# Kernel tuning notes

Hardware: AMD Instinct MI355X
Metric: run time of the kernel (lower is better)

## Reference

```python
import jax, jax.numpy as jnp
import numpy as np


def setup_inputs() -> dict:
    key = jax.random.key(0)
    k1, k2 = jax.random.split(key)
    B, C, L, K = 32, 64, 4096, 512
    inputs = jax.random.normal(k1, (B, C, L), dtype=jnp.float32)
    # codebook init: uniform(-1/K, 1/K) as in the torch module
    embed = jax.random.uniform(k2, (K, C), dtype=jnp.float32, minval=-1.0 / K, maxval=1.0 / K)
    return {"inputs": inputs, "embed": embed}


def reference(inputs, embed):
    commitment_cost = 0.25
    b, c, l = inputs.shape
    K = embed.shape[0]
    # (B, C, L) -> (B*L, C)
    flat = jnp.transpose(inputs, (0, 2, 1)).reshape(-1, c)
    flat_sq = jnp.sum(flat * flat, axis=1, keepdims=True)            # (N, 1)
    embed_sq = jnp.sum(embed * embed, axis=1)                        # (K,)
    distances = flat_sq + embed_sq[None, :] - 2.0 * (flat @ embed.T)  # (N, K)
    encoding_indices = jnp.argmin(distances, axis=1)                 # (N,)
    encodings = jax.nn.one_hot(encoding_indices, K, dtype=flat.dtype)  # (N, K)
    # gather codewords (equivalent to one_hot @ embed) and restore (B, C, L)
    quantized = jnp.transpose(embed[encoding_indices].reshape(b, l, c), (0, 2, 1))
    e_latent_loss = jnp.mean((jax.lax.stop_gradient(quantized) - inputs) ** 2)
    q_latent_loss = jnp.mean((quantized - jax.lax.stop_gradient(inputs)) ** 2)
    loss = q_latent_loss + commitment_cost * e_latent_loss
    # straight-through estimator
    quantized_st = inputs + jax.lax.stop_gradient(quantized - inputs)
    avg_probs = jnp.mean(encodings, axis=0)                          # (K,)
    perplexity = jnp.exp(-jnp.sum(avg_probs * jnp.log(avg_probs + 1e-10)))
    return (loss, quantized_st, perplexity, embed, encoding_indices.reshape(b, l), encodings)
```

## Files before the change

### kernel.cpp

```cpp
#include <hip/hip_runtime.h>
#include <math.h>

#define B_DIM 32
#define C_DIM 64
#define L_DIM 4096
#define K_CB  512
#define N_ROWS (B_DIM * L_DIM)
#define Q_ELEMS (B_DIM * C_DIM * L_DIM)

#define OFF_LOSS  0
#define OFF_Q     1
#define OFF_PERP  (1 + Q_ELEMS)
#define OFF_EMBED (OFF_PERP + 1)
#define OFF_IDX   (OFF_EMBED + K_CB * C_DIM)
#define OFF_ENC   (OFF_IDX + N_ROWS)

#define TM 128
#define KC 128

using f4 = __attribute__((ext_vector_type(4))) float;
using f2 = __attribute__((ext_vector_type(2))) float;


__global__ void vq_init(const float* __restrict__ embed,
                        double* __restrict__ loss_ws,
                        int* __restrict__ hist,
                        float* __restrict__ esq,
                        float* __restrict__ out_embed) {
  const int t = threadIdx.x;
  if (t == 0) *loss_ws = 0.0;
  hist[t] = 0;
  const float* row = embed + (size_t)t * C_DIM;
  float s = 0.f;
#pragma unroll
  for (int c = 0; c < C_DIM; ++c) s = fmaf(row[c], row[c], s);
  esq[t] = s;
#pragma unroll
  for (int i = 0; i < K_CB * C_DIM / 512; ++i)
    out_embed[i * 512 + t] = embed[i * 512 + t];
}

__global__ __launch_bounds__(256) void vq_fused(
    const float* __restrict__ in, const float* __restrict__ embed,
    const float* __restrict__ esq_g, int* __restrict__ hist,
    double* __restrict__ loss_ws, float* __restrict__ out) {
  __shared__ float xT[C_DIM][TM];
  __shared__ float eT[KC][C_DIM];
  __shared__ int   idx_s[TM];
  __shared__ double red[256];

  const int tid = threadIdx.x;
  const int blk = blockIdx.x;
  const int b   = blk >> 5;
  const int l0  = (blk & 31) * TM;
  const float* xbase = in + (size_t)b * C_DIM * L_DIM + l0;

  {
    const int rr = (tid & 31) * 4;
    const int c0 = tid >> 5;
#pragma unroll
    for (int p = 0; p < 8; ++p) {
      const int c = c0 * 8 + p;
      const f4 v = *(const f4*)(xbase + (size_t)c * L_DIM + rr);
      *(f4*)&xT[c][rr] = v;
    }
  }
  __syncthreads();

  const int tx = tid & 15;
  const int ty = tid >> 4;

  float* fsq_tmp = &eT[0][0];
  if (tid < TM) {
    float s = 0.f;
#pragma unroll
    for (int c = 0; c < C_DIM; ++c) { const float v = xT[c][tid]; s = fmaf(v, v, s); }
    fsq_tmp[tid] = s;
  }
  __syncthreads();
  float fs[8];
#pragma unroll
  for (int i = 0; i < 8; ++i) fs[i] = fsq_tmp[ty * 8 + i];

  const int swz = (tx & 7) << 2;
  float rmin[8];
  int   ridx[8];
#pragma unroll
  for (int i = 0; i < 8; ++i) { rmin[i] = 3.402823466e38f; ridx[i] = 0; }

  for (int kc = 0; kc < K_CB / KC; ++kc) {
    const int k0 = kc * KC;
    __syncthreads();
    {
      const int cg  = (tid & 15) * 4;
      const int kk0 = tid >> 4;
#pragma unroll
      for (int p = 0; p < 8; ++p) {
        const int kk = kk0 + p * 16;
        const f4 v = *(const f4*)(embed + (size_t)(k0 + kk) * C_DIM + cg);
        const int cs = cg ^ (((kk >> 3) & 7) << 2);
        *(f4*)&eT[kk][cs] = v;
      }
    }
    __syncthreads();

    float qe[8];
#pragma unroll
    for (int j = 0; j < 8; ++j) qe[j] = esq_g[k0 + tx * 8 + j];

    float acc[8][8];
#pragma unroll
    for (int i = 0; i < 8; ++i)
#pragma unroll
      for (int j = 0; j < 8; ++j) acc[i][j] = 0.f;

#pragma unroll 2
    for (int c = 0; c < C_DIM; c += 4) {
      f4 xa[4], xb[4], ev[8];
#pragma unroll
      for (int cc = 0; cc < 4; ++cc) {
        xa[cc] = *(const f4*)&xT[c + cc][ty * 8];
        xb[cc] = *(const f4*)&xT[c + cc][ty * 8 + 4];
      }
      const int cb = c ^ swz;
#pragma unroll
      for (int j = 0; j < 8; ++j)
        ev[j] = *(const f4*)&eT[tx * 8 + j][cb];
#pragma unroll
      for (int cc = 0; cc < 4; ++cc) {
#pragma unroll
        for (int j = 0; j < 8; ++j) {
          const float e = ev[j][cc];
#pragma unroll
          for (int i = 0; i < 4; ++i) acc[i][j]     = fmaf(xa[cc][i], e, acc[i][j]);
#pragma unroll
          for (int i = 0; i < 4; ++i) acc[i + 4][j] = fmaf(xb[cc][i], e, acc[i + 4][j]);
        }
      }
    }

#pragma unroll
    for (int i = 0; i < 8; ++i) {
#pragma unroll
      for (int j = 0; j < 8; ++j) {
        const float d = fmaf(-2.0f, acc[i][j], fs[i] + qe[j]);
        const int k = k0 + tx * 8 + j;
        if (d < rmin[i]) { rmin[i] = d; ridx[i] = k; }
      }
    }
  }

#pragma unroll
  for (int off = 8; off; off >>= 1) {
#pragma unroll
    for (int i = 0; i < 8; ++i) {
      const float od = __shfl_xor(rmin[i], off, 16);
      const int   oi = __shfl_xor(ridx[i], off, 16);
      if (od < rmin[i] || (od == rmin[i] && oi < ridx[i])) { rmin[i] = od; ridx[i] = oi; }
    }
  }

  if (tx == 0) {
#pragma unroll
    for (int i = 0; i < 8; ++i) idx_s[ty * 8 + i] = ridx[i];
  }
  __syncthreads();

  if (tid < TM) {
    const int k = idx_s[tid];
    out[OFF_IDX + blk * TM + tid] = (float)k;
    atomicAdd(&hist[k], 1);
  }

  {
    float* eSel = &eT[0][0];
    const int c = tid & 63;
    const int w = tid >> 6;
#pragma unroll 4
    for (int it = 0; it < 32; ++it) {
      const int r = it * 4 + w;
      const int k = idx_s[r];
      eSel[r * C_DIM + (c ^ (r & 31))] = embed[(size_t)k * C_DIM + c];
    }
  }
  __syncthreads();

  double ls = 0.0;
  {
    const float* eSel = &eT[0][0];
    float* qbase = out + OFF_Q + (size_t)b * (C_DIM * L_DIM) + l0;
#pragma unroll 4
    for (int it = 0; it < 32; ++it) {
      const int f = it * 256 + tid;
      const int c = f >> 7;
      const int r = f & 127;
      const float x = xT[c][r];
      const float q = eSel[r * C_DIM + (c ^ (r & 31))];
      const float d = q - x;
      __builtin_nontemporal_store(x + d, qbase + (size_t)c * L_DIM + r);
      ls += (double)(d * d);
    }
  }

  {
    f2* enc = (f2*)(out + OFF_ENC) + (size_t)blk * TM * (K_CB / 2);
#pragma unroll 4
    for (int it = 0; it < 128; ++it) {
      const int g = it * 256 + tid;
      const int row = g >> 8;
      const int j2 = (g & 255) << 1;
      const int k = idx_s[row];
      f2 v;
      v.x = (j2 == k)     ? 1.0f : 0.0f;
      v.y = (j2 + 1 == k) ? 1.0f : 0.0f;
      __builtin_nontemporal_store(v, enc + g);
    }
  }

  red[tid] = ls;
  __syncthreads();
  for (int s = 128; s; s >>= 1) {
    if (tid < s) red[tid] += red[tid + s];
    __syncthreads();
  }
  if (tid == 0) atomicAdd(loss_ws, red[0]);
}

__global__ void vq_final(const int* __restrict__ hist, const double* __restrict__ loss_ws,
                         float* __restrict__ out) {
  __shared__ float red[512];
  const int t = threadIdx.x;
  const float p = (float)hist[t] * (1.0f / (float)N_ROWS);
  red[t] = p * logf(p + 1e-10f);
  __syncthreads();
  for (int s = 256; s; s >>= 1) {
    if (t < s) red[t] += red[t + s];
    __syncthreads();
  }
  if (t == 0) {
    out[OFF_PERP] = expf(-red[0]);
    const float m = (float)(*loss_ws / (double)Q_ELEMS);
    out[OFF_LOSS] = m + 0.25f * m;
  }
}

extern "C" void kernel_launch(void* const* d_in, const int* in_sizes, int n_in,
                              void* d_out, int out_size, void* d_ws, size_t ws_size,
                              hipStream_t stream) {
  (void)in_sizes; (void)n_in; (void)out_size; (void)ws_size;
  const float* in    = (const float*)d_in[0];
  const float* embed = (const float*)d_in[1];
  float* out = (float*)d_out;

  double* loss_ws = (double*)d_ws;
  int*    hist    = (int*)((char*)d_ws + 16);
  float*  esq     = (float*)((char*)d_ws + 4096);

  vq_init<<<1, 512, 0, stream>>>(embed, loss_ws, hist, esq, out + OFF_EMBED);
  vq_fused<<<N_ROWS / TM, 256, 0, stream>>>(in, embed, esq, hist, loss_ws, out);
  vq_final<<<1, 512, 0, stream>>>(hist, loss_ws, out);
}
```

Before: 170.5 us.

## Halve codebook chunk, register-prefetch embed tiles, split gather into two passes

Shrinks the codebook chunk from 128 to 64 entries, which halves the eT shared buffer and cuts the accumulator tile to 8x4 per thread. The point is to lower LDS and register use so more blocks fit per CU. The next chunk of embed is prefetched into registers while the current one is processed, and the swizzle is widened to 16 groups to match the new layout. The codeword gather/writeback epilogue now runs in two 64-row passes so it fits the smaller buffer, and the one-hot store loop is simplified. In exchange the main loop runs twice as many iterations with their barriers, and each thread reuses its x loads across fewer codewords.

```diff
diff --git a/kernel.cpp b/kernel.cpp
--- a/kernel.cpp
+++ b/kernel.cpp
@@ -16,7 +16,7 @@
 #define OFF_ENC   (OFF_IDX + N_ROWS)
 
 #define TM 128
-#define KC 128
+#define KC 64
 
 using f4 = __attribute__((ext_vector_type(4))) float;
 using f2 = __attribute__((ext_vector_type(2))) float;
@@ -65,6 +65,14 @@
       *(f4*)&xT[c][rr] = v;
     }
   }
+
+  const int cg  = (tid & 15) * 4;
+  const int kk0 = tid >> 4;
+  f4 pf[4];
+#pragma unroll
+  for (int p = 0; p < 4; ++p)
+    pf[p] = *(const f4*)(embed + (size_t)(kk0 + p * 16) * C_DIM + cg);
+
   __syncthreads();
 
   const int tx = tid & 15;
@@ -82,7 +90,7 @@
 #pragma unroll
   for (int i = 0; i < 8; ++i) fs[i] = fsq_tmp[ty * 8 + i];
 
-  const int swz = (tx & 7) << 2;
+  const int swz = tx << 2;
   float rmin[8];
   int   ridx[8];
 #pragma unroll
@@ -91,32 +99,31 @@
   for (int kc = 0; kc < K_CB / KC; ++kc) {
     const int k0 = kc * KC;
     __syncthreads();
-    {
-      const int cg  = (tid & 15) * 4;
-      const int kk0 = tid >> 4;
-#pragma unroll
-      for (int p = 0; p < 8; ++p) {
-        const int kk = kk0 + p * 16;
-        const f4 v = *(const f4*)(embed + (size_t)(k0 + kk) * C_DIM + cg);
-        const int cs = cg ^ (((kk >> 3) & 7) << 2);
-        *(f4*)&eT[kk][cs] = v;
-      }
-    }
-    __syncthreads();
-
-    float qe[8];
-#pragma unroll
-    for (int j = 0; j < 8; ++j) qe[j] = esq_g[k0 + tx * 8 + j];
-
-    float acc[8][8];
+#pragma unroll
+    for (int p = 0; p < 4; ++p) {
+      const int kk = kk0 + p * 16;
+      const int cs = cg ^ (((kk >> 2) & 15) << 2);
+      *(f4*)&eT[kk][cs] = pf[p];
+    }
+    if (kc < K_CB / KC - 1) {
+#pragma unroll
+      for (int p = 0; p < 4; ++p)
+        pf[p] = *(const f4*)(embed + (size_t)(k0 + KC + kk0 + p * 16) * C_DIM + cg);
+    }
+    float qe[4];
+#pragma unroll
+    for (int j = 0; j < 4; ++j) qe[j] = esq_g[k0 + tx * 4 + j];
+    __syncthreads();
+
+    float acc[8][4];
 #pragma unroll
     for (int i = 0; i < 8; ++i)
 #pragma unroll
-      for (int j = 0; j < 8; ++j) acc[i][j] = 0.f;
+      for (int j = 0; j < 4; ++j) acc[i][j] = 0.f;
 
 #pragma unroll 2
     for (int c = 0; c < C_DIM; c += 4) {
-      f4 xa[4], xb[4], ev[8];
+      f4 xa[4], xb[4], ev[4];
 #pragma unroll
       for (int cc = 0; cc < 4; ++cc) {
         xa[cc] = *(const f4*)&xT[c + cc][ty * 8];
@@ -124,12 +131,12 @@
       }
       const int cb = c ^ swz;
 #pragma unroll
-      for (int j = 0; j < 8; ++j)
-        ev[j] = *(const f4*)&eT[tx * 8 + j][cb];
+      for (int j = 0; j < 4; ++j)
+        ev[j] = *(const f4*)&eT[tx * 4 + j][cb];
 #pragma unroll
       for (int cc = 0; cc < 4; ++cc) {
 #pragma unroll
-        for (int j = 0; j < 8; ++j) {
+        for (int j = 0; j < 4; ++j) {
           const float e = ev[j][cc];
 #pragma unroll
           for (int i = 0; i < 4; ++i) acc[i][j]     = fmaf(xa[cc][i], e, acc[i][j]);
@@ -142,9 +149,9 @@
 #pragma unroll
     for (int i = 0; i < 8; ++i) {
 #pragma unroll
-      for (int j = 0; j < 8; ++j) {
+      for (int j = 0; j < 4; ++j) {
         const float d = fmaf(-2.0f, acc[i][j], fs[i] + qe[j]);
-        const int k = k0 + tx * 8 + j;
+        const int k = k0 + tx * 4 + j;
         if (d < rmin[i]) { rmin[i] = d; ridx[i] = k; }
       }
     }
@@ -172,48 +179,47 @@
     atomicAdd(&hist[k], 1);
   }
 
+  double ls = 0.0;
   {
     float* eSel = &eT[0][0];
-    const int c = tid & 63;
-    const int w = tid >> 6;
+    float* qbase = out + OFF_Q + (size_t)b * (C_DIM * L_DIM) + l0;
+    const int cc = tid & 63;
+    const int w  = tid >> 6;
+#pragma unroll
+    for (int pass = 0; pass < 2; ++pass) {
+      const int r0 = pass * 64;
+      __syncthreads();
 #pragma unroll 4
-    for (int it = 0; it < 32; ++it) {
-      const int r = it * 4 + w;
-      const int k = idx_s[r];
-      eSel[r * C_DIM + (c ^ (r & 31))] = embed[(size_t)k * C_DIM + c];
-    }
-  }
-  __syncthreads();
-
-  double ls = 0.0;
-  {
-    const float* eSel = &eT[0][0];
-    float* qbase = out + OFF_Q + (size_t)b * (C_DIM * L_DIM) + l0;
+      for (int it = 0; it < 16; ++it) {
+        const int r = it * 4 + w;
+        const int k = idx_s[r0 + r];
+        eSel[r * C_DIM + (cc ^ (r & 31))] = embed[(size_t)k * C_DIM + cc];
+      }
+      __syncthreads();
 #pragma unroll 4
-    for (int it = 0; it < 32; ++it) {
-      const int f = it * 256 + tid;
-      const int c = f >> 7;
-      const int r = f & 127;
-      const float x = xT[c][r];
-      const float q = eSel[r * C_DIM + (c ^ (r & 31))];
-      const float d = q - x;
-      __builtin_nontemporal_store(x + d, qbase + (size_t)c * L_DIM + r);
-      ls += (double)(d * d);
+      for (int it = 0; it < 16; ++it) {
+        const int f = it * 256 + tid;
+        const int c = f >> 6;
+        const int r = f & 63;
+        const float x = xT[c][r0 + r];
+        const float q = eSel[r * C_DIM + (c ^ (r & 31))];
+        const float d = q - x;
+        __builtin_nontemporal_store(x + d, qbase + (size_t)c * L_DIM + r0 + r);
+        ls += (double)(d * d);
+      }
     }
   }
 
   {
     f2* enc = (f2*)(out + OFF_ENC) + (size_t)blk * TM * (K_CB / 2);
 #pragma unroll 4
-    for (int it = 0; it < 128; ++it) {
-      const int g = it * 256 + tid;
-      const int row = g >> 8;
-      const int j2 = (g & 255) << 1;
-      const int k = idx_s[row];
+    for (int it = 0; it < TM; ++it) {
+      const int k = idx_s[it];
+      const int j2 = tid << 1;
       f2 v;
       v.x = (j2 == k)     ? 1.0f : 0.0f;
       v.y = (j2 + 1 == k) ? 1.0f : 0.0f;
-      __builtin_nontemporal_store(v, enc + g);
+      __builtin_nontemporal_store(v, enc + it * 256 + tid);
     }
   }
 
```

Measured after the change: 167.6 us. About the same (-1.7%).
